# Kernel optimization log

Measured on AMD Instinct MI355X. Metric: run time of the kernel, lower is better.

Reference implementation:

```python
import jax, jax.numpy as jnp
import numpy as np

B, S, H = 1, 2048, 1024
NH, HD = 16, 64          # num heads, head dim (H = NH*HD)
NT = 1024                # param token num (qkv_slot_num = proj_slot_num)


def pattention(x, key_tokens, value_tokens):
    """Pattention with gelu_l2_norm: x:[...,H] -> [...,out]."""
    attn = jnp.einsum('bsh,th->bst', x, key_tokens)          # scale_factor = 1
    g = jax.nn.gelu(attn, approximate=False)                 # torch F.gelu exact
    norm = jnp.linalg.norm(g, axis=-1, keepdims=True)
    w = g / norm * jnp.sqrt(jnp.asarray(g.shape[-1], g.dtype))
    return jnp.einsum('bst,td->bsd', w, value_tokens)


def setup_inputs() -> dict:
    key = jax.random.key(0)
    ks = jax.random.split(key, 9)
    names = ['q_key', 'q_val', 'k_key', 'k_val', 'v_key', 'v_val', 'proj_key', 'proj_val']
    inp = {'x': jax.random.normal(ks[0], (B, S, H), jnp.float32)}
    for i, n in enumerate(names):
        inp[n] = jax.random.normal(ks[i + 1], (NT, H), jnp.float32) * 0.02
    return inp


def reference(x, q_key, q_val, k_key, k_val, v_key, v_val, proj_key, proj_val):
    # Q/K/V via Pattention (token-parameter attention)
    q = pattention(x, q_key, q_val).reshape(B, S, NH, HD)
    k = pattention(x, k_key, k_val).reshape(B, S, NH, HD)
    v = pattention(x, v_key, v_val).reshape(B, S, NH, HD)
    # causal softmax attention, scale = 1/sqrt(head_dim) (flash default)
    scale = 1.0 / jnp.sqrt(jnp.asarray(HD, q.dtype))
    scores = jnp.einsum('bqhd,bkhd->bhqk', q, k) * scale
    causal = jnp.tril(jnp.ones((S, S), dtype=bool))
    scores = jnp.where(causal, scores, jnp.asarray(-1e30, scores.dtype))
    probs = jax.nn.softmax(scores, axis=-1)
    ctx = jnp.einsum('bhqk,bkhd->bqhd', probs, v).reshape(B, S, H)
    # output projection via Pattention
    return pattention(ctx, proj_key, proj_val)
```

## Files before the change

### kernel.cpp

```cpp
#include <hip/hip_runtime.h>
#include <cstdint>
#include <cstddef>

#define S_LEN 2048
#define H_DIM 1024
#define NTOK  1024
#define NHEAD 16
#define HDIM  64
#define NSPLIT 4

typedef __bf16 bf16;
typedef __bf16 bf16x8 __attribute__((ext_vector_type(8)));
typedef __bf16 bf16x4 __attribute__((ext_vector_type(4)));
typedef float  f32x4  __attribute__((ext_vector_type(4)));

static __device__ __forceinline__ f32x4 mfma16(bf16x8 a, bf16x8 b, f32x4 c) {
    return __builtin_amdgcn_mfma_f32_16x16x32_bf16(a, b, c, 0, 0, 0);
}

static __device__ __forceinline__ void async16(const void* gp, void* lp) {
    __builtin_amdgcn_global_load_lds(
        (const __attribute__((address_space(1))) void*)gp,
        (__attribute__((address_space(3))) void*)lp, 16, 0, 0);
}

struct ConvArgs {
    const float* src[6];
    bf16* dst[6];
};
__global__ __launch_bounds__(256) void convert6(ConvArgs a) {
    const float* __restrict__ s = a.src[blockIdx.y];
    bf16* __restrict__ d = a.dst[blockIdx.y];
    size_t i = ((size_t)blockIdx.x * 256 + threadIdx.x) * 4;
    f32x4 v = *(const f32x4*)&s[i];
    bf16x4 o;
    o[0] = (bf16)v[0]; o[1] = (bf16)v[1]; o[2] = (bf16)v[2]; o[3] = (bf16)v[3];
    *(bf16x4*)&d[i] = o;
}

struct TcArgs {
    const float* src[4];
    bf16* dst[4];
};
__global__ void transpose_cvt(TcArgs a) {
    const float* __restrict__ in = a.src[blockIdx.z];
    bf16* __restrict__ out = a.dst[blockIdx.z];
    __shared__ float t[32][33];
    const int bx = blockIdx.x * 32, by = blockIdx.y * 32;
    const int x = threadIdx.x, y = threadIdx.y;
#pragma unroll
    for (int j = 0; j < 32; j += 8)
        t[y + j][x] = in[(size_t)(by + y + j) * 1024 + bx + x];
    __syncthreads();
#pragma unroll
    for (int j = 0; j < 32; j += 8)
        out[(size_t)(bx + y + j) * 1024 + by + x] = (bf16)t[x][y + j];
}

__global__ __launch_bounds__(256) void vtrans_kernel(const bf16* __restrict__ V,
                                                     bf16* __restrict__ Vt) {
    const int k0 = blockIdx.x * 64, h = blockIdx.y;
    const int tid = threadIdx.x;
    __shared__ __align__(16) bf16 tile[64 * 64];
    const int kk = tid >> 3, d8 = (tid & 7) * 8;
#pragma unroll
    for (int p = 0; p < 2; ++p) {
        int k = kk + p * 32;
        bf16x8 v = *(const bf16x8*)&V[(size_t)(k0 + k) * H_DIM + h * 64 + d8];
#pragma unroll
        for (int e = 0; e < 8; ++e)
            tile[(d8 + e) * 64 + (k ^ ((d8 + e) & 56))] = v[e];
    }
    __syncthreads();
    const int d = tid >> 2;
#pragma unroll
    for (int c = 0; c < 2; ++c) {
        int k8 = ((tid & 3) * 2 + c) * 8;
        bf16x8 v = *(const bf16x8*)&tile[d * 64 + (k8 ^ (d & 56))];
        int pos = (((k8 >> 3) ^ (d & 7)) << 3);
        *(bf16x8*)&Vt[((size_t)(h * 64 + d)) * 2048 + k0 + pos] = v;
    }
}

template <int MODE, typename OutT>
struct GemmArgs {
    const bf16* A[3];
    const bf16* B[3];
    OutT* C[3];
    const float* S[3];
};

template <int MODE, typename OutT>
__global__ __launch_bounds__(256, 2) void gemm_bt128(GemmArgs<MODE, OutT> args) {
    constexpr int Kd = 1024, Nd = 1024, BK = 64;
    const bf16* __restrict__ A = args.A[blockIdx.z];
    const bf16* __restrict__ B = args.B[blockIdx.z];
    OutT* __restrict__ C = args.C[blockIdx.z];
    const float* __restrict__ S = args.S[blockIdx.z];

    __shared__ __align__(16) bf16 As[2][128 * BK];
    __shared__ __align__(16) bf16 Bs[2][128 * BK];

    const int tid = threadIdx.x;
    const int w = tid >> 6, lane = tid & 63, quad = lane >> 4, m16 = lane & 15;
    const int wm = (w >> 1) * 64, wn = (w & 1) * 64;
    const int bm = blockIdx.y * 128, bn = blockIdx.x * 128;

    const int srow = lane >> 3;
    const int sseg = ((lane & 7) ^ srow) * 8;

    auto stage = [&](int buf, int k0) {
        const bf16* Ab = A + (size_t)bm * Kd + k0;
        const bf16* Bb = B + (size_t)bn * Kd + k0;
#pragma unroll
        for (int c = 0; c < 4; ++c) {
            int chunk = w * 4 + c;
            async16(Ab + (size_t)(chunk * 8 + srow) * Kd + sseg,
                    &As[buf][chunk * 512]);
            async16(Bb + (size_t)(chunk * 8 + srow) * Kd + sseg,
                    &Bs[buf][chunk * 512]);
        }
    };

    f32x4 acc[4][4] = {};
    stage(0, 0);

    for (int k0 = 0; k0 < Kd; k0 += BK) {
        const int buf = (k0 >> 6) & 1;
        asm volatile("s_waitcnt vmcnt(0)" ::: "memory");
        __syncthreads();
        if (k0 + BK < Kd) stage(buf ^ 1, k0 + BK);

        bf16x8 a[2][4], b[2][4];
#pragma unroll
        for (int kc = 0; kc < 2; ++kc) {
#pragma unroll
            for (int i = 0; i < 4; ++i) {
                int row = wm + i * 16 + m16;
                a[kc][i] = *(const bf16x8*)
                    &As[buf][row * 64 + (((kc * 4 + quad) ^ (row & 7)) << 3)];
            }
#pragma unroll
            for (int j = 0; j < 4; ++j) {
                int row = wn + j * 16 + m16;
                b[kc][j] = *(const bf16x8*)
                    &Bs[buf][row * 64 + (((kc * 4 + quad) ^ (row & 7)) << 3)];
            }
        }
#pragma unroll
        for (int kc = 0; kc < 2; ++kc)
#pragma unroll
            for (int i = 0; i < 4; ++i)
#pragma unroll
                for (int j = 0; j < 4; ++j)
                    acc[i][j] = mfma16(a[kc][i], b[kc][j], acc[i][j]);
    }

#pragma unroll
    for (int i = 0; i < 4; ++i)
#pragma unroll
        for (int j = 0; j < 4; ++j)
#pragma unroll
            for (int r = 0; r < 4; ++r) {
                int row = bm + wm + i * 16 + quad * 4 + r;
                int col = bn + wn + j * 16 + m16;
                float v = acc[i][j][r];
                if (MODE == 1)
                    v = 0.5f * v * (1.0f + erff(v * 0.70710678118654752f));
                if (MODE == 2) v *= S[row];
                C[(size_t)row * Nd + col] = (OutT)v;
            }
}

template <int MODE, typename OutT>
__global__ __launch_bounds__(256, 3) void gemm_bt64(GemmArgs<MODE, OutT> args) {
    constexpr int Kd = 1024, Nd = 1024, BK = 64;
    const bf16* __restrict__ A = args.A[blockIdx.z];
    const bf16* __restrict__ B = args.B[blockIdx.z];
    OutT* __restrict__ C = args.C[blockIdx.z];
    const float* __restrict__ S = args.S[blockIdx.z];

    __shared__ __align__(16) bf16 As[2][128 * BK];
    __shared__ __align__(16) bf16 Bs[2][64 * BK];

    const int tid = threadIdx.x;
    const int w = tid >> 6, lane = tid & 63, quad = lane >> 4, m16 = lane & 15;
    const int wm = (w >> 1) * 64, wn = (w & 1) * 32;
    const int bm = blockIdx.y * 128, bn = blockIdx.x * 64;

    const int srow = lane >> 3;
    const int sseg = ((lane & 7) ^ srow) * 8;

    auto stage = [&](int buf, int k0) {
        const bf16* Ab = A + (size_t)bm * Kd + k0;
#pragma unroll
        for (int c = 0; c < 4; ++c) {
            int chunk = w * 4 + c;
            async16(Ab + (size_t)(chunk * 8 + srow) * Kd + sseg,
                    &As[buf][chunk * 512]);
        }
        const bf16* Bb = B + (size_t)bn * Kd + k0;
#pragma unroll
        for (int c = 0; c < 2; ++c) {
            int chunk = w * 2 + c;
            async16(Bb + (size_t)(chunk * 8 + srow) * Kd + sseg,
                    &Bs[buf][chunk * 512]);
        }
    };

    f32x4 acc[4][2] = {};
    stage(0, 0);

    for (int k0 = 0; k0 < Kd; k0 += BK) {
        const int buf = (k0 >> 6) & 1;
        asm volatile("s_waitcnt vmcnt(0)" ::: "memory");
        __syncthreads();
        if (k0 + BK < Kd) stage(buf ^ 1, k0 + BK);

        bf16x8 a[2][4], b[2][2];
#pragma unroll
        for (int kc = 0; kc < 2; ++kc) {
#pragma unroll
            for (int i = 0; i < 4; ++i) {
                int row = wm + i * 16 + m16;
                a[kc][i] = *(const bf16x8*)
                    &As[buf][row * 64 + (((kc * 4 + quad) ^ (row & 7)) << 3)];
            }
#pragma unroll
            for (int j = 0; j < 2; ++j) {
                int row = wn + j * 16 + m16;
                b[kc][j] = *(const bf16x8*)
                    &Bs[buf][row * 64 + (((kc * 4 + quad) ^ (row & 7)) << 3)];
            }
        }
#pragma unroll
        for (int kc = 0; kc < 2; ++kc)
#pragma unroll
            for (int i = 0; i < 4; ++i)
#pragma unroll
                for (int j = 0; j < 2; ++j)
                    acc[i][j] = mfma16(a[kc][i], b[kc][j], acc[i][j]);
    }

#pragma unroll
    for (int i = 0; i < 4; ++i)
#pragma unroll
        for (int j = 0; j < 2; ++j)
#pragma unroll
            for (int r = 0; r < 4; ++r) {
                int row = bm + wm + i * 16 + quad * 4 + r;
                int col = bn + wn + j * 16 + m16;
                float v = acc[i][j][r];
                if (MODE == 1)
                    v = 0.5f * v * (1.0f + erff(v * 0.70710678118654752f));
                if (MODE == 2) v *= S[row];
                C[(size_t)row * Nd + col] = (OutT)v;
            }
}

struct ScaleArgs { const bf16* G[3]; float* S[3]; };
__global__ __launch_bounds__(256) void rowscale_kernel(ScaleArgs a) {
    __shared__ float wsum[4];
    const bf16* __restrict__ G = a.G[blockIdx.y];
    float* __restrict__ S = a.S[blockIdx.y];
    const int row = blockIdx.x, tid = threadIdx.x;
    bf16x4 g = *(const bf16x4*)&G[(size_t)row * 1024 + tid * 4];
    float f0 = (float)g[0], f1 = (float)g[1], f2 = (float)g[2], f3 = (float)g[3];
    float ss = f0 * f0 + f1 * f1 + f2 * f2 + f3 * f3;
#pragma unroll
    for (int sh = 1; sh < 64; sh <<= 1) ss += __shfl_xor(ss, sh);
    if ((tid & 63) == 0) wsum[tid >> 6] = ss;
    __syncthreads();
    if (tid == 0) {
        float total = wsum[0] + wsum[1] + wsum[2] + wsum[3];
        S[row] = 32.0f * rsqrtf(total);
    }
}

struct FlashArgs {
    const bf16* Q;
    const bf16* K;
    const bf16* VtG;
    bf16* op[NSPLIT];
    float* ml;
};

__global__ __launch_bounds__(256, 4) void flash_kernel(FlashArgs fa) {
    const int pr = blockIdx.x, h = blockIdx.y, s = blockIdx.z;
    const int tid = threadIdx.x;
    const int w = tid >> 6, lane = tid & 63, quad = lane >> 4, m16 = lane & 15;
    const int hOff = h * HDIM;

    __shared__ __align__(16) bf16 Vs[64 * 64];
    __shared__ __align__(16) bf16 Pw[4][16][72];

    const int vrow = tid >> 3, vchunk = (tid & 7) * 8;
    const bf16* VtH = fa.VtG + (size_t)hOff * 2048;
    bf16* __restrict__ Opart = fa.op[s];

#pragma unroll
    for (int ti = 0; ti < 2; ++ti) {
        const int qt = ti ? 31 - pr : pr;
        const int qRow = qt * 64 + w * 16 + m16;
        bf16x8 bq[2];
        bq[0] = *(const bf16x8*)&fa.Q[(size_t)qRow * H_DIM + hOff + quad * 8];
        bq[1] = *(const bf16x8*)&fa.Q[(size_t)qRow * H_DIM + hOff + 32 + quad * 8];

        f32x4 oacc[4] = {};
        float m_i = -1e30f, l_i = 0.0f;

        for (int kt = s; kt <= qt; kt += NSPLIT) {
            const int k0 = kt * 64;
            const bool diag = (kt == qt);
            __syncthreads();
#pragma unroll
            for (int p = 0; p < 2; ++p) {
                int d = vrow + p * 32;
                async16(VtH + (size_t)d * 2048 + k0 + vchunk,
                        &Vs[d * 64 + vchunk]);
            }
            f32x4 sacc[4] = {};
#pragma unroll
            for (int ks = 0; ks < 2; ++ks)
#pragma unroll
                for (int j = 0; j < 4; ++j) {
                    bf16x8 ak = *(const bf16x8*)
                        &fa.K[(size_t)(k0 + j * 16 + m16) * H_DIM + hOff +
                              ks * 32 + quad * 8];
                    sacc[j] = mfma16(ak, bq[ks], sacc[j]);
                }
            float sv[4][4];
            float mx = -1e30f;
#pragma unroll
            for (int j = 0; j < 4; ++j)
#pragma unroll
                for (int rr = 0; rr < 4; ++rr) {
                    float sc = sacc[j][rr] * 0.125f;
                    int kcol = k0 + j * 16 + quad * 4 + rr;
                    if (diag && kcol > qRow) sc = -1e30f;
                    sv[j][rr] = sc;
                    mx = fmaxf(mx, sc);
                }
            mx = fmaxf(mx, __shfl_xor(mx, 16));
            mx = fmaxf(mx, __shfl_xor(mx, 32));
            float mnew = fmaxf(m_i, mx);
            float alpha = __expf(m_i - mnew);
            m_i = mnew;
            float ls = 0.0f;
#pragma unroll
            for (int j = 0; j < 4; ++j) {
                bf16x4 pk;
#pragma unroll
                for (int rr = 0; rr < 4; ++rr) {
                    float p = __expf(sv[j][rr] - mnew);
                    ls += p;
                    pk[rr] = (bf16)p;
                }
                *(bf16x4*)&Pw[w][m16][j * 16 + quad * 4] = pk;
            }
            ls += __shfl_xor(ls, 16);
            ls += __shfl_xor(ls, 32);
            l_i = l_i * alpha + ls;
#pragma unroll
            for (int jd = 0; jd < 4; ++jd)
#pragma unroll
                for (int rr = 0; rr < 4; ++rr) oacc[jd][rr] *= alpha;
            asm volatile("s_waitcnt vmcnt(0)" ::: "memory");
            __syncthreads();
#pragma unroll
            for (int ks = 0; ks < 2; ++ks) {
                bf16x8 bp = *(const bf16x8*)&Pw[w][m16][ks * 32 + quad * 8];
#pragma unroll
                for (int jd = 0; jd < 4; ++jd) {
                    int d = jd * 16 + m16;
                    bf16x8 av = *(const bf16x8*)
                        &Vs[d * 64 + (((ks * 4 + quad) ^ (d & 7)) << 3)];
                    oacc[jd] = mfma16(av, bp, oacc[jd]);
                }
            }
        }
#pragma unroll
        for (int jd = 0; jd < 4; ++jd) {
            bf16x4 o4;
#pragma unroll
            for (int rr = 0; rr < 4; ++rr) o4[rr] = (bf16)oacc[jd][rr];
            *(bf16x4*)&Opart[(size_t)qRow * 1024 + hOff + jd * 16 + quad * 4] = o4;
        }
        if (quad == 0) {
            float* p = fa.ml + ((size_t)(s * 2048 + qRow) * 16 + h) * 2;
            p[0] = m_i;
            p[1] = l_i;
        }
    }
}

struct CombArgs {
    const bf16* op[NSPLIT];
    const float* ml;
    bf16* ctx;
};
__global__ __launch_bounds__(256) void combine_kernel(CombArgs ca) {
    const int unit = blockIdx.x * 4 + (threadIdx.x >> 6);
    const int row = unit >> 4, h = unit & 15;
    const int d = threadIdx.x & 63;
    float mv[NSPLIT], lv[NSPLIT], M = -1e30f;
#pragma unroll
    for (int s2 = 0; s2 < NSPLIT; ++s2) {
        const float* p = ca.ml + ((size_t)(s2 * 2048 + row) * 16 + h) * 2;
        mv[s2] = p[0];
        lv[s2] = p[1];
        M = fmaxf(M, mv[s2]);
    }
    float num = 0.0f, den = 0.0f;
#pragma unroll
    for (int s2 = 0; s2 < NSPLIT; ++s2) {
        float e = __expf(mv[s2] - M);
        den += lv[s2] * e;
        num += e * (float)ca.op[s2][(size_t)row * 1024 + h * 64 + d];
    }
    ca.ctx[(size_t)row * 1024 + h * 64 + d] = (bf16)(num / den);
}

extern "C" void kernel_launch(void* const* d_in, const int* in_sizes, int n_in,
                              void* d_out, int out_size, void* d_ws,
                              size_t ws_size, hipStream_t stream) {
    const float* x = (const float*)d_in[0];
    const float* keysF[4] = {(const float*)d_in[1], (const float*)d_in[3],
                             (const float*)d_in[5], (const float*)d_in[7]};
    const float* valsF[4] = {(const float*)d_in[2], (const float*)d_in[4],
                             (const float*)d_in[6], (const float*)d_in[8]};
    float* out = (float*)d_out;

    char* ws = (char*)d_ws;
    bf16* xb = (bf16*)(ws);
    bf16* g3[3];
    for (int i = 0; i < 3; ++i) g3[i] = (bf16*)(ws + (4ull << 20) + (size_t)i * (4ull << 20));
    bf16* kb16[4], *vT16[4];
    for (int i = 0; i < 4; ++i) {
        kb16[i] = (bf16*)(ws + (16ull << 20) + (size_t)i * (2ull << 20));
        vT16[i] = (bf16*)(ws + (24ull << 20) + (size_t)i * (2ull << 20));
    }
    bf16* qb    = (bf16*)(ws);
    bf16* kbuf  = (bf16*)(ws + (32ull << 20));
    bf16* vbuf  = (bf16*)(ws + (36ull << 20));
    float* mlbuf = (float*)(ws + (20ull << 20));
    float* Sbuf = (float*)(ws + (20ull << 20) + (1536ull << 10));
    bf16* VtG   = (bf16*)(ws + (24ull << 20));
    bf16* ctx   = (bf16*)(ws + (32ull << 20));
    bf16* projg = (bf16*)(ws + (4ull << 20));

    bf16* opart[NSPLIT];
    for (int i = 0; i < NSPLIT; ++i)
        opart[i] = (bf16*)(ws + (4ull << 20) + (size_t)i * (4ull << 20));

    ConvArgs cva;
    cva.src[0] = x;             cva.dst[0] = xb;
    cva.src[1] = x + (1 << 20); cva.dst[1] = xb + (1 << 20);
    for (int i = 0; i < 4; ++i) { cva.src[2 + i] = keysF[i]; cva.dst[2 + i] = kb16[i]; }
    convert6<<<dim3(1024, 6), 256, 0, stream>>>(cva);

    TcArgs ta;
    for (int i = 0; i < 4; ++i) { ta.src[i] = valsF[i]; ta.dst[i] = vT16[i]; }
    transpose_cvt<<<dim3(32, 32, 4), dim3(32, 8), 0, stream>>>(ta);

    GemmArgs<1, bf16> g1;
    for (int z = 0; z < 3; ++z) {
        g1.A[z] = xb; g1.B[z] = kb16[z]; g1.C[z] = g3[z]; g1.S[z] = nullptr;
    }
    gemm_bt128<1, bf16><<<dim3(8, 16, 3), 256, 0, stream>>>(g1);

    ScaleArgs sa;
    for (int z = 0; z < 3; ++z) { sa.G[z] = g3[z]; sa.S[z] = Sbuf + z * 2048; }
    rowscale_kernel<<<dim3(2048, 3), 256, 0, stream>>>(sa);

    GemmArgs<2, bf16> g2;
    bf16* qkv[3] = {qb, kbuf, vbuf};
    for (int z = 0; z < 3; ++z) {
        g2.A[z] = g3[z]; g2.B[z] = vT16[z]; g2.C[z] = qkv[z]; g2.S[z] = Sbuf + z * 2048;
    }
    gemm_bt128<2, bf16><<<dim3(8, 16, 3), 256, 0, stream>>>(g2);

    vtrans_kernel<<<dim3(32, 16), 256, 0, stream>>>(vbuf, VtG);

    FlashArgs fla;
    fla.Q = qb; fla.K = kbuf; fla.VtG = VtG; fla.ml = mlbuf;
    for (int i = 0; i < NSPLIT; ++i) fla.op[i] = opart[i];
    flash_kernel<<<dim3(16, 16, NSPLIT), 256, 0, stream>>>(fla);

    CombArgs cba;
    for (int i = 0; i < NSPLIT; ++i) cba.op[i] = opart[i];
    cba.ml = mlbuf; cba.ctx = ctx;
    combine_kernel<<<dim3(8192), 256, 0, stream>>>(cba);

    GemmArgs<1, bf16> p1;
    for (int z = 0; z < 3; ++z) {
        p1.A[z] = ctx; p1.B[z] = kb16[3]; p1.C[z] = projg; p1.S[z] = nullptr;
    }
    gemm_bt64<1, bf16><<<dim3(16, 16, 1), 256, 0, stream>>>(p1);

    ScaleArgs sp;
    for (int z = 0; z < 3; ++z) { sp.G[z] = projg; sp.S[z] = Sbuf; }
    rowscale_kernel<<<dim3(2048, 1), 256, 0, stream>>>(sp);

    GemmArgs<2, float> p2;
    for (int z = 0; z < 3; ++z) {
        p2.A[z] = projg; p2.B[z] = vT16[3]; p2.C[z] = out; p2.S[z] = Sbuf;
    }
    gemm_bt64<2, float><<<dim3(16, 16, 1), 256, 0, stream>>>(p2);
}
```

Baseline: 251.6 us.

## Fuse V transpose into GEMM epilogue, shrink GEMM tiles, remap flash grid

The V-projection GEMM now writes its result directly in the swizzled transposed layout used by flash attention, so the separate vtrans kernel and the intermediate V buffer go away. The QKV GEMMs move from 128x128 to 128x64 tiles with more blocks and higher occupancy. The projection GEMMs run on a 512-thread variant with smaller per-wave tiles. The flash kernel uses a flattened 1D grid that interleaves heads to change block scheduling and cache locality. Smaller tiles re-read more operand data, and the transposed epilogue does scattered 8-byte stores.

```diff
diff --git a/kernel.cpp b/kernel.cpp
--- a/kernel.cpp
+++ b/kernel.cpp
@@ -57,72 +57,53 @@
         out[(size_t)(bx + y + j) * 1024 + by + x] = (bf16)t[x][y + j];
 }
 
-__global__ __launch_bounds__(256) void vtrans_kernel(const bf16* __restrict__ V,
-                                                     bf16* __restrict__ Vt) {
-    const int k0 = blockIdx.x * 64, h = blockIdx.y;
-    const int tid = threadIdx.x;
-    __shared__ __align__(16) bf16 tile[64 * 64];
-    const int kk = tid >> 3, d8 = (tid & 7) * 8;
-#pragma unroll
-    for (int p = 0; p < 2; ++p) {
-        int k = kk + p * 32;
-        bf16x8 v = *(const bf16x8*)&V[(size_t)(k0 + k) * H_DIM + h * 64 + d8];
-#pragma unroll
-        for (int e = 0; e < 8; ++e)
-            tile[(d8 + e) * 64 + (k ^ ((d8 + e) & 56))] = v[e];
-    }
-    __syncthreads();
-    const int d = tid >> 2;
-#pragma unroll
-    for (int c = 0; c < 2; ++c) {
-        int k8 = ((tid & 3) * 2 + c) * 8;
-        bf16x8 v = *(const bf16x8*)&tile[d * 64 + (k8 ^ (d & 56))];
-        int pos = (((k8 >> 3) ^ (d & 7)) << 3);
-        *(bf16x8*)&Vt[((size_t)(h * 64 + d)) * 2048 + k0 + pos] = v;
-    }
-}
-
 template <int MODE, typename OutT>
 struct GemmArgs {
     const bf16* A[3];
     const bf16* B[3];
     OutT* C[3];
     const float* S[3];
+    bf16* Ct[3];
 };
 
 template <int MODE, typename OutT>
-__global__ __launch_bounds__(256, 2) void gemm_bt128(GemmArgs<MODE, OutT> args) {
+__global__ __launch_bounds__(256, 3) void gemm_bt(GemmArgs<MODE, OutT> args) {
     constexpr int Kd = 1024, Nd = 1024, BK = 64;
     const bf16* __restrict__ A = args.A[blockIdx.z];
     const bf16* __restrict__ B = args.B[blockIdx.z];
     OutT* __restrict__ C = args.C[blockIdx.z];
     const float* __restrict__ S = args.S[blockIdx.z];
+    bf16* __restrict__ Ct = args.Ct[blockIdx.z];
 
     __shared__ __align__(16) bf16 As[2][128 * BK];
-    __shared__ __align__(16) bf16 Bs[2][128 * BK];
+    __shared__ __align__(16) bf16 Bs[2][64 * BK];
 
     const int tid = threadIdx.x;
     const int w = tid >> 6, lane = tid & 63, quad = lane >> 4, m16 = lane & 15;
-    const int wm = (w >> 1) * 64, wn = (w & 1) * 64;
-    const int bm = blockIdx.y * 128, bn = blockIdx.x * 128;
+    const int wm = (w >> 1) * 64, wn = (w & 1) * 32;
+    const int bm = blockIdx.y * 128, bn = blockIdx.x * 64;
 
     const int srow = lane >> 3;
     const int sseg = ((lane & 7) ^ srow) * 8;
 
     auto stage = [&](int buf, int k0) {
         const bf16* Ab = A + (size_t)bm * Kd + k0;
-        const bf16* Bb = B + (size_t)bn * Kd + k0;
 #pragma unroll
         for (int c = 0; c < 4; ++c) {
             int chunk = w * 4 + c;
             async16(Ab + (size_t)(chunk * 8 + srow) * Kd + sseg,
                     &As[buf][chunk * 512]);
+        }
+        const bf16* Bb = B + (size_t)bn * Kd + k0;
+#pragma unroll
+        for (int c = 0; c < 2; ++c) {
+            int chunk = w * 2 + c;
             async16(Bb + (size_t)(chunk * 8 + srow) * Kd + sseg,
                     &Bs[buf][chunk * 512]);
         }
     };
 
-    f32x4 acc[4][4] = {};
+    f32x4 acc[4][2] = {};
     stage(0, 0);
 
     for (int k0 = 0; k0 < Kd; k0 += BK) {
@@ -131,7 +112,7 @@
         __syncthreads();
         if (k0 + BK < Kd) stage(buf ^ 1, k0 + BK);
 
-        bf16x8 a[2][4], b[2][4];
+        bf16x8 a[2][4], b[2][2];
 #pragma unroll
         for (int kc = 0; kc < 2; ++kc) {
 #pragma unroll
@@ -141,7 +122,7 @@
                     &As[buf][row * 64 + (((kc * 4 + quad) ^ (row & 7)) << 3)];
             }
 #pragma unroll
-            for (int j = 0; j < 4; ++j) {
+            for (int j = 0; j < 2; ++j) {
                 int row = wn + j * 16 + m16;
                 b[kc][j] = *(const bf16x8*)
                     &Bs[buf][row * 64 + (((kc * 4 + quad) ^ (row & 7)) << 3)];
@@ -152,14 +133,32 @@
 #pragma unroll
             for (int i = 0; i < 4; ++i)
 #pragma unroll
-                for (int j = 0; j < 4; ++j)
+                for (int j = 0; j < 2; ++j)
                     acc[i][j] = mfma16(a[kc][i], b[kc][j], acc[i][j]);
     }
 
+    if (MODE == 2 && Ct != nullptr) {
+#pragma unroll
+        for (int i = 0; i < 4; ++i)
+#pragma unroll
+            for (int j = 0; j < 2; ++j) {
+                int k = bm + wm + i * 16 + quad * 4;
+                int col = bn + wn + j * 16 + m16;
+                bf16x4 o4;
+#pragma unroll
+                for (int r = 0; r < 4; ++r)
+                    o4[r] = (bf16)(acc[i][j][r] * S[k + r]);
+                int kb = k >> 6, c = (k >> 3) & 7, off = k & 7;
+                int pos = ((c ^ (col & 7)) << 3) + off;
+                *(bf16x4*)&Ct[(size_t)col * 2048 + kb * 64 + pos] = o4;
+            }
+        return;
+    }
+
 #pragma unroll
     for (int i = 0; i < 4; ++i)
 #pragma unroll
-        for (int j = 0; j < 4; ++j)
+        for (int j = 0; j < 2; ++j)
 #pragma unroll
             for (int r = 0; r < 4; ++r) {
                 int row = bm + wm + i * 16 + quad * 4 + r;
@@ -173,7 +172,7 @@
 }
 
 template <int MODE, typename OutT>
-__global__ __launch_bounds__(256, 3) void gemm_bt64(GemmArgs<MODE, OutT> args) {
+__global__ __launch_bounds__(512) void gemm_bt512(GemmArgs<MODE, OutT> args) {
     constexpr int Kd = 1024, Nd = 1024, BK = 64;
     const bf16* __restrict__ A = args.A[blockIdx.z];
     const bf16* __restrict__ B = args.B[blockIdx.z];
@@ -185,7 +184,7 @@
 
     const int tid = threadIdx.x;
     const int w = tid >> 6, lane = tid & 63, quad = lane >> 4, m16 = lane & 15;
-    const int wm = (w >> 1) * 64, wn = (w & 1) * 32;
+    const int wm = (w >> 1) * 32, wn = (w & 1) * 32;
     const int bm = blockIdx.y * 128, bn = blockIdx.x * 64;
 
     const int srow = lane >> 3;
@@ -194,21 +193,20 @@
     auto stage = [&](int buf, int k0) {
         const bf16* Ab = A + (size_t)bm * Kd + k0;
 #pragma unroll
-        for (int c = 0; c < 4; ++c) {
-            int chunk = w * 4 + c;
+        for (int c = 0; c < 2; ++c) {
+            int chunk = w * 2 + c;
             async16(Ab + (size_t)(chunk * 8 + srow) * Kd + sseg,
                     &As[buf][chunk * 512]);
         }
         const bf16* Bb = B + (size_t)bn * Kd + k0;
-#pragma unroll
-        for (int c = 0; c < 2; ++c) {
-            int chunk = w * 2 + c;
+        {
+            int chunk = w;
             async16(Bb + (size_t)(chunk * 8 + srow) * Kd + sseg,
                     &Bs[buf][chunk * 512]);
         }
     };
 
-    f32x4 acc[4][2] = {};
+    f32x4 acc[2][2] = {};
     stage(0, 0);
 
     for (int k0 = 0; k0 < Kd; k0 += BK) {
@@ -217,11 +215,11 @@
         __syncthreads();
         if (k0 + BK < Kd) stage(buf ^ 1, k0 + BK);
 
-        bf16x8 a[2][4], b[2][2];
+        bf16x8 a[2][2], b[2][2];
 #pragma unroll
         for (int kc = 0; kc < 2; ++kc) {
 #pragma unroll
-            for (int i = 0; i < 4; ++i) {
+            for (int i = 0; i < 2; ++i) {
                 int row = wm + i * 16 + m16;
                 a[kc][i] = *(const bf16x8*)
                     &As[buf][row * 64 + (((kc * 4 + quad) ^ (row & 7)) << 3)];
@@ -236,14 +234,14 @@
 #pragma unroll
         for (int kc = 0; kc < 2; ++kc)
 #pragma unroll
-            for (int i = 0; i < 4; ++i)
+            for (int i = 0; i < 2; ++i)
 #pragma unroll
                 for (int j = 0; j < 2; ++j)
                     acc[i][j] = mfma16(a[kc][i], b[kc][j], acc[i][j]);
     }
 
 #pragma unroll
-    for (int i = 0; i < 4; ++i)
+    for (int i = 0; i < 2; ++i)
 #pragma unroll
         for (int j = 0; j < 2; ++j)
 #pragma unroll
@@ -286,7 +284,11 @@
 };
 
 __global__ __launch_bounds__(256, 4) void flash_kernel(FlashArgs fa) {
-    const int pr = blockIdx.x, h = blockIdx.y, s = blockIdx.z;
+    const int bid = blockIdx.x;
+    const int idx = bid >> 3;
+    const int h = (bid & 7) * 2 + (idx & 1);
+    const int pr = (idx >> 1) & 15;
+    const int s = idx >> 5;
     const int tid = threadIdx.x;
     const int w = tid >> 6, lane = tid & 63, quad = lane >> 4, m16 = lane & 15;
     const int hOff = h * HDIM;
@@ -442,10 +444,9 @@
     }
     bf16* qb    = (bf16*)(ws);
     bf16* kbuf  = (bf16*)(ws + (32ull << 20));
-    bf16* vbuf  = (bf16*)(ws + (36ull << 20));
     float* mlbuf = (float*)(ws + (20ull << 20));
     float* Sbuf = (float*)(ws + (20ull << 20) + (1536ull << 10));
-    bf16* VtG   = (bf16*)(ws + (24ull << 20));
+    bf16* VtG   = (bf16*)(ws + (36ull << 20));
     bf16* ctx   = (bf16*)(ws + (32ull << 20));
     bf16* projg = (bf16*)(ws + (4ull << 20));
 
@@ -465,27 +466,28 @@
 
     GemmArgs<1, bf16> g1;
     for (int z = 0; z < 3; ++z) {
-        g1.A[z] = xb; g1.B[z] = kb16[z]; g1.C[z] = g3[z]; g1.S[z] = nullptr;
-    }
-    gemm_bt128<1, bf16><<<dim3(8, 16, 3), 256, 0, stream>>>(g1);
+        g1.A[z] = xb; g1.B[z] = kb16[z]; g1.C[z] = g3[z];
+        g1.S[z] = nullptr; g1.Ct[z] = nullptr;
+    }
+    gemm_bt<1, bf16><<<dim3(16, 16, 3), 256, 0, stream>>>(g1);
 
     ScaleArgs sa;
     for (int z = 0; z < 3; ++z) { sa.G[z] = g3[z]; sa.S[z] = Sbuf + z * 2048; }
     rowscale_kernel<<<dim3(2048, 3), 256, 0, stream>>>(sa);
 
     GemmArgs<2, bf16> g2;
-    bf16* qkv[3] = {qb, kbuf, vbuf};
+    bf16* qkv[3] = {qb, kbuf, qb };
     for (int z = 0; z < 3; ++z) {
-        g2.A[z] = g3[z]; g2.B[z] = vT16[z]; g2.C[z] = qkv[z]; g2.S[z] = Sbuf + z * 2048;
-    }
-    gemm_bt128<2, bf16><<<dim3(8, 16, 3), 256, 0, stream>>>(g2);
-
-    vtrans_kernel<<<dim3(32, 16), 256, 0, stream>>>(vbuf, VtG);
+        g2.A[z] = g3[z]; g2.B[z] = vT16[z]; g2.C[z] = qkv[z];
+        g2.S[z] = Sbuf + z * 2048;
+        g2.Ct[z] = (z == 2) ? VtG : nullptr;
+    }
+    gemm_bt<2, bf16><<<dim3(16, 16, 3), 256, 0, stream>>>(g2);
 
     FlashArgs fla;
     fla.Q = qb; fla.K = kbuf; fla.VtG = VtG; fla.ml = mlbuf;
     for (int i = 0; i < NSPLIT; ++i) fla.op[i] = opart[i];
-    flash_kernel<<<dim3(16, 16, NSPLIT), 256, 0, stream>>>(fla);
+    flash_kernel<<<dim3(1024), 256, 0, stream>>>(fla);
 
     CombArgs cba;
     for (int i = 0; i < NSPLIT; ++i) cba.op[i] = opart[i];
@@ -494,9 +496,10 @@
 
     GemmArgs<1, bf16> p1;
     for (int z = 0; z < 3; ++z) {
-        p1.A[z] = ctx; p1.B[z] = kb16[3]; p1.C[z] = projg; p1.S[z] = nullptr;
-    }
-    gemm_bt64<1, bf16><<<dim3(16, 16, 1), 256, 0, stream>>>(p1);
+        p1.A[z] = ctx; p1.B[z] = kb16[3]; p1.C[z] = projg;
+        p1.S[z] = nullptr; p1.Ct[z] = nullptr;
+    }
+    gemm_bt512<1, bf16><<<dim3(16, 16, 1), 512, 0, stream>>>(p1);
 
     ScaleArgs sp;
     for (int z = 0; z < 3; ++z) { sp.G[z] = projg; sp.S[z] = Sbuf; }
@@ -504,7 +507,8 @@
 
     GemmArgs<2, float> p2;
     for (int z = 0; z < 3; ++z) {
-        p2.A[z] = projg; p2.B[z] = vT16[3]; p2.C[z] = out; p2.S[z] = Sbuf;
-    }
-    gemm_bt64<2, float><<<dim3(16, 16, 1), 256, 0, stream>>>(p2);
-}
+        p2.A[z] = projg; p2.B[z] = vT16[3]; p2.C[z] = out;
+        p2.S[z] = Sbuf; p2.Ct[z] = nullptr;
+    }
+    gemm_bt512<2, float><<<dim3(16, 16, 1), 512, 0, stream>>>(p2);
+}
```

New measurement: 237.3 us. 1.06x faster.
